# Optimization experiments

Measured on AMD Instinct MI355X. Metric: run time of the kernel, lower is better.

The kernel has to match this reference:

```python
import jax, jax.numpy as jnp
import numpy as np

DIM = 256
H = 56
W = 56
WS = 7          # window_size
SHIFT = 3       # shift_size = WS // 2
NH = 8          # num_heads
HID = 4 * DIM   # mlp hidden
EPS = 1e-5
N = WS * WS     # tokens per window


def _rel_coords_table():
    # SwinV2 continuous log-spaced relative coords, pretrained_window_size=0
    r = np.arange(-(WS - 1), WS, dtype=np.float32)
    t = np.stack(np.meshgrid(r, r, indexing='ij'), axis=-1)[None]  # (1, 2WS-1, 2WS-1, 2)
    t = t / (WS - 1) * 8.0
    t = np.sign(t) * np.log2(np.abs(t) + 1.0) / np.log2(8.0)
    return jnp.asarray(t, jnp.float32)


def _rel_pos_index():
    coords = np.stack(np.meshgrid(np.arange(WS), np.arange(WS), indexing='ij'))  # (2, WS, WS)
    cf = coords.reshape(2, -1)
    rel = (cf[:, :, None] - cf[:, None, :]).transpose(1, 2, 0).astype(np.int64)  # (N, N, 2)
    rel[..., 0] += WS - 1
    rel[..., 1] += WS - 1
    rel[..., 0] *= 2 * WS - 1
    return jnp.asarray(rel.sum(-1), jnp.int32)  # (N, N)


def _attn_mask():
    # shifted-window mask: -100 where tokens come from different image regions
    img = np.zeros((1, H, W, 1), np.float32)
    cnt = 0
    for hs in (slice(0, -WS), slice(-WS, -SHIFT), slice(-SHIFT, None)):
        for ws_ in (slice(0, -WS), slice(-WS, -SHIFT), slice(-SHIFT, None)):
            img[:, hs, ws_, :] = cnt
            cnt += 1
    mw = img.reshape(1, H // WS, WS, W // WS, WS, 1).transpose(0, 1, 3, 2, 4, 5).reshape(-1, N)
    m = mw[:, None, :] - mw[:, :, None]
    return jnp.asarray(np.where(m != 0, -100.0, 0.0).astype(np.float32))  # (nW, N, N)


def _win_partition(x):  # (B, H, W, C) -> (B*nW, N, C)
    B, _, _, C = x.shape
    x = x.reshape(B, H // WS, WS, W // WS, WS, C).transpose(0, 1, 3, 2, 4, 5)
    return x.reshape(-1, N, C)


def _win_reverse(w, B):  # (B*nW, N, C) -> (B, H, W, C)
    C = w.shape[-1]
    x = w.reshape(B, H // WS, W // WS, WS, WS, C).transpose(0, 1, 3, 2, 4, 5)
    return x.reshape(B, H, W, C)


def _ln(x, g, b):
    mu = jnp.mean(x, axis=-1, keepdims=True)
    var = jnp.mean(jnp.square(x - mu), axis=-1, keepdims=True)
    return (x - mu) * jax.lax.rsqrt(var + EPS) * g + b


def setup_inputs() -> dict:
    key = jax.random.key(0)
    ks = jax.random.split(key, 16)
    s = lambda fan: 1.0 / np.sqrt(fan)
    return {
        'x': jax.random.normal(ks[0], (16, H * W, DIM), jnp.float32),
        'norm1_w': jnp.ones((DIM,), jnp.float32),
        'norm1_b': jnp.zeros((DIM,), jnp.float32),
        'qkv_w': jax.random.normal(ks[1], (3 * DIM, DIM), jnp.float32) * s(DIM),
        'q_bias': jnp.zeros((DIM,), jnp.float32),
        'v_bias': jnp.zeros((DIM,), jnp.float32),
        'logit_scale': jnp.full((NH, 1, 1), np.log(10.0), jnp.float32),
        'cpb_w1': jax.random.normal(ks[2], (512, 2), jnp.float32) * s(2),
        'cpb_b1': jnp.zeros((512,), jnp.float32),
        'cpb_w2': jax.random.normal(ks[3], (NH, 512), jnp.float32) * s(512),
        'proj_w': jax.random.normal(ks[4], (DIM, DIM), jnp.float32) * s(DIM),
        'proj_b': jnp.zeros((DIM,), jnp.float32),
        'norm2_w': jnp.ones((DIM,), jnp.float32),
        'norm2_b': jnp.zeros((DIM,), jnp.float32),
        'fc1_w': jax.random.normal(ks[5], (HID, DIM), jnp.float32) * s(DIM),
        'fc1_b': jnp.zeros((HID,), jnp.float32),
        'fc2_w': jax.random.normal(ks[6], (DIM, HID), jnp.float32) * s(HID),
        'fc2_b': jnp.zeros((DIM,), jnp.float32),
    }


def reference(x, norm1_w, norm1_b, qkv_w, q_bias, v_bias, logit_scale,
              cpb_w1, cpb_b1, cpb_w2, proj_w, proj_b,
              norm2_w, norm2_b, fc1_w, fc1_b, fc2_w, fc2_b):
    B, L, C = x.shape
    hd = C // NH
    shortcut = x

    # cyclic shift + window partition
    xs = jnp.roll(x.reshape(B, H, W, C), (-SHIFT, -SHIFT), axis=(1, 2))
    xw = _win_partition(xs)  # (B*nW, N, C)

    # qkv with q/v bias, zero k bias (SwinV2)
    qkv_b = jnp.concatenate([q_bias, jnp.zeros_like(q_bias), v_bias])
    qkv = (xw @ qkv_w.T + qkv_b).reshape(-1, N, 3, NH, hd).transpose(2, 0, 3, 1, 4)
    q, k, v = qkv[0], qkv[1], qkv[2]  # (B*nW, NH, N, hd)

    # cosine attention with clamped learned logit scale
    qn = q / jnp.maximum(jnp.linalg.norm(q, axis=-1, keepdims=True), 1e-12)
    kn = k / jnp.maximum(jnp.linalg.norm(k, axis=-1, keepdims=True), 1e-12)
    scale = jnp.exp(jnp.minimum(logit_scale, jnp.log(jnp.asarray(100.0, x.dtype))))
    attn = jnp.einsum('whnd,whmd->whnm', qn, kn) * scale[None]

    # continuous relative position bias via cpb MLP
    t = _rel_coords_table()  # (1, 2WS-1, 2WS-1, 2)
    tbl = (jax.nn.relu(t @ cpb_w1.T + cpb_b1) @ cpb_w2.T).reshape(-1, NH)
    rpb = tbl[_rel_pos_index().reshape(-1)].reshape(N, N, NH).transpose(2, 0, 1)
    attn = attn + (16.0 * jax.nn.sigmoid(rpb))[None]

    # shifted-window mask
    mask = _attn_mask()  # (nW, N, N)
    nW = mask.shape[0]
    attn = attn.reshape(B, nW, NH, N, N) + mask[None, :, None]
    attn = jax.nn.softmax(attn, axis=-1).reshape(-1, NH, N, N)

    out = jnp.einsum('whnm,whmd->whnd', attn, v).transpose(0, 2, 1, 3).reshape(-1, N, C)
    out = out @ proj_w.T + proj_b

    # reverse windows + reverse shift (SwinV2 post-norm residual)
    xs = jnp.roll(_win_reverse(out, B), (SHIFT, SHIFT), axis=(1, 2)).reshape(B, L, C)
    x = shortcut + _ln(xs, norm1_w, norm1_b)

    # MLP with tanh-approx GELU (matches Triton kernel), post-norm residual
    hmid = jax.nn.gelu(x @ fc1_w.T + fc1_b, approximate=True)
    mlp = hmid @ fc2_w.T + fc2_b
    return x + _ln(mlp, norm2_w, norm2_b)
```

## Files before the change

### kernel.cpp

```cpp
#include <hip/hip_runtime.h>
#include <hip/hip_bf16.h>

typedef __attribute__((ext_vector_type(8))) short short8;
typedef __attribute__((ext_vector_type(4))) float f32x4;

union I4S8 { int4 i; short8 s; };

#if defined(__has_builtin)
#if __has_builtin(__builtin_amdgcn_global_load_lds)
#define HAVE_GLL 1
#endif
#endif

__device__ __forceinline__ unsigned short f2b(float f) {
  union { __hip_bfloat16 h; unsigned short u; } c;
  c.h = __float2bfloat16(f);
  return c.u;
}
__device__ __forceinline__ unsigned pk2(float a, float b) {
  union { __hip_bfloat162 h2; unsigned u; } c;
  c.h2 = __hip_bfloat162{__float2bfloat16(a), __float2bfloat16(b)};
  return c.u;
}
__device__ __forceinline__ float b2f(unsigned short h) {
  return __uint_as_float(((unsigned)h) << 16);
}
__device__ __forceinline__ float gelu_fast(float v) {
  float c2 = 1.5957691216057308f * (v + 0.044715f * v * v * v);
  return v / (1.0f + __expf(-c2));
}

__device__ __forceinline__ void stage8(const unsigned short* ga, unsigned short* lds_base,
                                       int lane) {
#ifdef HAVE_GLL
  __builtin_amdgcn_global_load_lds(
      (const __attribute__((address_space(1))) void*)ga,
      (__attribute__((address_space(3))) void*)lds_base, 16, 0, 0);
#else
  *(int4*)(lds_base + (lane >> 3) * 64 + (lane & 7) * 8) = *(const int4*)ga;
#endif
}

__global__ void k_misc(const float* __restrict__ logit_scale,
                       const float* __restrict__ w1, const float* __restrict__ b1,
                       const float* __restrict__ w2,
                       float* __restrict__ scales, float* __restrict__ tblg) {
  const int bb = blockIdx.x;
  const int t = threadIdx.x;
  if (bb == 169) {
    if (t < 8) scales[t] = expf(fminf(logit_scale[t], logf(100.0f)));
    return;
  }
  __shared__ float red[4][8];
  int a = bb / 13, b = bb % 13;
  float ra = (float)(a - 6) * (8.0f / 6.0f);
  float rb = (float)(b - 6) * (8.0f / 6.0f);
  float sa = (ra > 0.f) ? 1.f : ((ra < 0.f) ? -1.f : 0.f);
  float sb = (rb > 0.f) ? 1.f : ((rb < 0.f) ? -1.f : 0.f);
  float t0 = sa * log2f(fabsf(ra) + 1.0f) / 3.0f;
  float t1 = sb * log2f(fabsf(rb) + 1.0f) / 3.0f;
  float acc[8];
#pragma unroll
  for (int hh = 0; hh < 8; ++hh) acc[hh] = 0.f;
#pragma unroll
  for (int jj = 0; jj < 2; ++jj) {
    int j = t + jj * 256;
    float hv = fmaxf(w1[2 * j] * t0 + w1[2 * j + 1] * t1 + b1[j], 0.0f);
#pragma unroll
    for (int hh = 0; hh < 8; ++hh) acc[hh] += w2[hh * 512 + j] * hv;
  }
#pragma unroll
  for (int hh = 0; hh < 8; ++hh) {
    acc[hh] += __shfl_xor(acc[hh], 1);
    acc[hh] += __shfl_xor(acc[hh], 2);
    acc[hh] += __shfl_xor(acc[hh], 4);
    acc[hh] += __shfl_xor(acc[hh], 8);
    acc[hh] += __shfl_xor(acc[hh], 16);
    acc[hh] += __shfl_xor(acc[hh], 32);
  }
  if ((t & 63) == 0) {
#pragma unroll
    for (int hh = 0; hh < 8; ++hh) red[t >> 6][hh] = acc[hh];
  }
  __syncthreads();
  if (t < 8) tblg[bb * 8 + t] = red[0][t] + red[1][t] + red[2][t] + red[3][t];
}

__global__ void k_bias(const float* __restrict__ tblg, float* __restrict__ biasT) {
  int idx = blockIdx.x * 256 + threadIdx.x;
  int h = idx >> 12, rem = idx & 4095, k = rem >> 6, q = rem & 63;
  float v;
  if (k >= 49 || q >= 49) {
    v = -3.0e8f;
  } else {
    int e = (q / 7 - k / 7 + 6) * 13 + (q % 7 - k % 7 + 6);
    float r = tblg[e * 8 + h];
    v = 16.0f / (1.0f + expf(-r));
  }
  biasT[idx] = v;
}

__global__ void k_cvt(const float* __restrict__ qkv_w, const float* __restrict__ proj_w,
                      const float* __restrict__ fc1_w, const float* __restrict__ fc2_w,
                      unsigned short* __restrict__ wq, unsigned short* __restrict__ wp,
                      unsigned short* __restrict__ w1, unsigned short* __restrict__ w2) {
  int i = blockIdx.x * 256 + threadIdx.x;
  if (i < 196608) wq[i] = f2b(qkv_w[i]);
  else if (i < 262144) wp[i - 196608] = f2b(proj_w[i - 196608]);
  else if (i < 524288) w1[i - 262144] = f2b(fc1_w[i - 262144]);
  else w2[i - 524288] = f2b(fc2_w[i - 524288]);
}

__global__ void k_xprep(const float* __restrict__ x, unsigned short* __restrict__ xw) {
  int id = blockIdx.x * 256 + threadIdx.x;
  int row = id >> 5, c8 = (id & 31) << 3;
  int win = row / 49, r = row - win * 49;
  int b = win >> 6, wi = (win >> 3) & 7, wj = win & 7;
  int i = r / 7, j = r - i * 7;
  int ho = (wi * 7 + i + 3) % 56;
  int wo = (wj * 7 + j + 3) % 56;
  const float* src = x + (size_t)(b * 3136 + ho * 56 + wo) * 256 + c8;
  float4 f0 = *(const float4*)(src);
  float4 f1 = *(const float4*)(src + 4);
  int4 pk;
  pk.x = pk2(f0.x, f0.y);
  pk.y = pk2(f0.z, f0.w);
  pk.z = pk2(f1.x, f1.y);
  pk.w = pk2(f1.z, f1.w);
  *(int4*)(xw + (size_t)row * 256 + c8) = pk;
}

__global__ void k_xb(const float* __restrict__ x1, unsigned short* __restrict__ xb) {
  int id = blockIdx.x * 256 + threadIdx.x;
  size_t off = (size_t)id << 3;
  const float* src = x1 + off;
  float4 f0 = *(const float4*)(src);
  float4 f1 = *(const float4*)(src + 4);
  int4 pk;
  pk.x = pk2(f0.x, f0.y);
  pk.y = pk2(f0.z, f0.w);
  pk.z = pk2(f1.x, f1.y);
  pk.w = pk2(f1.z, f1.w);
  *(int4*)(xb + off) = pk;
}

__launch_bounds__(512)
__global__ void k_qkvg(const unsigned short* __restrict__ xw, const unsigned short* __restrict__ wq,
                       const float* __restrict__ q_bias, const float* __restrict__ v_bias,
                       const float* __restrict__ scales, unsigned short* __restrict__ qkv) {
  const int mb = blockIdx.x, nb = blockIdx.y;
  const int t = threadIdx.x, lane = t & 63, w = t >> 6;
  const int wm = w >> 2, wn = w & 3;
  const int l15 = lane & 15, g = lane >> 4, rj = g << 2;

  __shared__ __align__(16) unsigned short As[128 * 64];
  __shared__ __align__(16) unsigned short Bs[256 * 64];

  f32x4 acc[4][4];
#pragma unroll
  for (int mf = 0; mf < 4; ++mf)
#pragma unroll
    for (int nf = 0; nf < 4; ++nf) acc[mf][nf] = (f32x4){0.f, 0.f, 0.f, 0.f};

  const int rl = lane >> 3;
  const int ca = (lane & 7) ^ rl;

  for (int kb = 0; kb < 4; ++kb) {
    __syncthreads();
#pragma unroll
    for (int i = 0; i < 6; ++i) {
      int gidx = w * 6 + i;
      if (gidx < 16) {
        int r = gidx * 8 + rl;
        stage8(xw + (size_t)(mb * 128 + r) * 256 + kb * 64 + ca * 8, As + gidx * 8 * 64, lane);
      } else {
        int gb = gidx - 16;
        int r = gb * 8 + rl;
        stage8(wq + (size_t)(nb * 256 + r) * 256 + kb * 64 + ca * 8, Bs + gb * 8 * 64, lane);
      }
    }
    __syncthreads();
#pragma unroll
    for (int ks = 0; ks < 2; ++ks) {
      short8 a_[4], b_[4];
#pragma unroll
      for (int mf = 0; mf < 4; ++mf) {
        int R = wm * 64 + mf * 16 + l15;
        a_[mf] = *(const short8*)(As + R * 64 + (((ks * 4 + g) ^ (R & 7)) << 3));
      }
#pragma unroll
      for (int nf = 0; nf < 4; ++nf) {
        int R = wn * 64 + nf * 16 + l15;
        b_[nf] = *(const short8*)(Bs + R * 64 + (((ks * 4 + g) ^ (R & 7)) << 3));
      }
#pragma unroll
      for (int mf = 0; mf < 4; ++mf)
#pragma unroll
        for (int nf = 0; nf < 4; ++nf)
          acc[mf][nf] = __builtin_amdgcn_mfma_f32_16x16x32_bf16(a_[mf], b_[nf], acc[mf][nf], 0, 0, 0);
    }
  }

  const int which = nb;
  if (which != 1) {
    const float* bp = (which == 0) ? q_bias : v_bias;
#pragma unroll
    for (int nf = 0; nf < 4; ++nf) {
      float bias = bp[wn * 64 + nf * 16 + l15];
#pragma unroll
      for (int mf = 0; mf < 4; ++mf)
#pragma unroll
        for (int j = 0; j < 4; ++j) acc[mf][nf][j] += bias;
    }
  }
  if (which < 2) {
#pragma unroll
    for (int mf = 0; mf < 4; ++mf)
#pragma unroll
      for (int p = 0; p < 2; ++p)
#pragma unroll
        for (int j = 0; j < 4; ++j) {
          float ss = acc[mf][2*p][j] * acc[mf][2*p][j] + acc[mf][2*p+1][j] * acc[mf][2*p+1][j];
          ss += __shfl_xor(ss, 1); ss += __shfl_xor(ss, 2);
          ss += __shfl_xor(ss, 4); ss += __shfl_xor(ss, 8);
          float inv = 1.0f / fmaxf(sqrtf(ss), 1e-12f);
          if (which == 0) inv *= scales[wn * 2 + p];
          acc[mf][2*p][j] *= inv;
          acc[mf][2*p+1][j] *= inv;
        }
  }
#pragma unroll
  for (int mf = 0; mf < 4; ++mf)
#pragma unroll
    for (int j = 0; j < 4; ++j) {
      int row_g = mb * 128 + wm * 64 + mf * 16 + rj + j;
      int win = row_g / 49, r = row_g - win * 49;
      size_t base = (((size_t)win * 3 + which) * 8) * 1568;
#pragma unroll
      for (int nf = 0; nf < 4; ++nf) {
        int h = wn * 2 + (nf >> 1), d = (nf & 1) * 16 + l15;
        qkv[base + (size_t)h * 1568 + r * 32 + d] = f2b(acc[mf][nf][j]);
      }
    }
}

__launch_bounds__(256, 4)
__global__ void k_attn2(unsigned short* __restrict__ qkv, const float* __restrict__ biasT) {
  const int win = blockIdx.x;
  const int wi = (win >> 3) & 7, wj = win & 7;
  const int t = threadIdx.x, lane = t & 63, w = t >> 6;
  const int l15 = lane & 15, g = lane >> 4;
  const int kk8 = g << 3, rj = g << 2;

  __shared__ __align__(16) unsigned short VT8[8 * 32 * 72];

  const int vi = (wi == 7) ? 1 : 0, vj = (wj == 7) ? 1 : 0;

  for (int idx = t; idx < 392; idx += 256) {
    int h = idx / 49, r = idx % 49;
    const unsigned short* vp = qkv + ((((size_t)win * 3 + 2) * 8 + h) * 49 + r) * 32;
    unsigned short vv[32];
    *(int4*)(vv + 0)  = *(const int4*)(vp + 0);
    *(int4*)(vv + 8)  = *(const int4*)(vp + 8);
    *(int4*)(vv + 16) = *(const int4*)(vp + 16);
    *(int4*)(vv + 24) = *(const int4*)(vp + 24);
    unsigned short* dst = VT8 + h * 2304;
#pragma unroll
    for (int d = 0; d < 32; ++d) dst[d * 72 + r] = vv[d];
  }
  for (int idx = t; idx < 3840; idx += 256) {
    int h = idx / 480, rem = idx % 480, d = rem / 15, r = 49 + rem % 15;
    VT8[h * 2304 + d * 72 + r] = 0;
  }
  __syncthreads();

  const int sA = l15 + ((g & 1) << 5);
  const int sB = sA + 16;
  const bool hi = ((g >> 1) & 1) != 0;

  unsigned ob[2][8][2];
  for (int hh = 0; hh < 2; ++hh) {
    const int h = w + hh * 4;
    const float* bT = biasT + (size_t)h * 4096;
    f32x4 s[4][4];
#pragma unroll
    for (int mf = 0; mf < 4; ++mf)
#pragma unroll
      for (int nf = 0; nf < 4; ++nf)
#pragma unroll
        for (int j = 0; j < 4; ++j)
          s[mf][nf][j] = bT[(mf * 16 + rj + j) * 64 + nf * 16 + l15];
    if (vi | vj) {
      int rq[4];
#pragma unroll
      for (int nf = 0; nf < 4; ++nf) {
        int q = nf * 16 + l15, qi = q / 7, qj = q - qi * 7;
        int aq = vi ? (qi < 4 ? 1 : 2) : 0;
        int bq = vj ? (qj < 4 ? 1 : 2) : 0;
        rq[nf] = aq * 3 + bq;
      }
#pragma unroll
      for (int mf = 0; mf < 4; ++mf)
#pragma unroll
        for (int j = 0; j < 4; ++j) {
          int k = mf * 16 + rj + j, ki = k / 7, kj = k - ki * 7;
          int ak = vi ? (ki < 4 ? 1 : 2) : 0;
          int bk = vj ? (kj < 4 ? 1 : 2) : 0;
          int rk = ak * 3 + bk;
#pragma unroll
          for (int nf = 0; nf < 4; ++nf)
            if (rq[nf] != rk) s[mf][nf][j] -= 100.0f;
        }
    }
    const unsigned short* kp = qkv + (((size_t)win * 3 + 1) * 8 + h) * 1568;
    const unsigned short* qp = qkv + (((size_t)win * 3 + 0) * 8 + h) * 1568;
    short8 ka[4], qa[4];
#pragma unroll
    for (int f = 0; f < 4; ++f) {
      ka[f] = *(const short8*)(kp + (f * 16 + l15) * 32 + kk8);
      qa[f] = *(const short8*)(qp + (f * 16 + l15) * 32 + kk8);
    }
#pragma unroll
    for (int mf = 0; mf < 4; ++mf)
#pragma unroll
      for (int nf = 0; nf < 4; ++nf)
        s[mf][nf] = __builtin_amdgcn_mfma_f32_16x16x32_bf16(ka[mf], qa[nf], s[mf][nf], 0, 0, 0);

    unsigned D[4][4][2];
#pragma unroll
    for (int nf = 0; nf < 4; ++nf) {
      float m = -3.0e8f;
#pragma unroll
      for (int mf = 0; mf < 4; ++mf)
#pragma unroll
        for (int j = 0; j < 4; ++j) m = fmaxf(m, s[mf][nf][j]);
      m = fmaxf(m, __shfl_xor(m, 16));
      m = fmaxf(m, __shfl_xor(m, 32));
      float sum = 0.f;
#pragma unroll
      for (int mf = 0; mf < 4; ++mf)
#pragma unroll
        for (int j = 0; j < 4; ++j) {
          float e = __expf(s[mf][nf][j] - m);
          s[mf][nf][j] = e; sum += e;
        }
      sum += __shfl_xor(sum, 16);
      sum += __shfl_xor(sum, 32);
      float inv = 1.0f / sum;
#pragma unroll
      for (int mf = 0; mf < 4; ++mf) {
        D[mf][nf][0] = pk2(s[mf][nf][0] * inv, s[mf][nf][1] * inv);
        D[mf][nf][1] = pk2(s[mf][nf][2] * inv, s[mf][nf][3] * inv);
      }
    }

    f32x4 o[8];
#pragma unroll
    for (int i = 0; i < 8; ++i) o[i] = (f32x4){0.f, 0.f, 0.f, 0.f};
#pragma unroll
    for (int ks = 0; ks < 2; ++ks) {
      short8 vb[2];
#pragma unroll
      for (int dt = 0; dt < 2; ++dt)
        vb[dt] = *(const short8*)(VT8 + h * 2304 + (dt * 16 + l15) * 72 + ks * 32 + kk8);
#pragma unroll
      for (int qt = 0; qt < 4; ++qt) {
        int a0 = __shfl((int)D[2*ks+0][qt][0], sA), a1 = __shfl((int)D[2*ks+1][qt][0], sA);
        int b0 = __shfl((int)D[2*ks+0][qt][1], sA), b1 = __shfl((int)D[2*ks+1][qt][1], sA);
        int c0 = __shfl((int)D[2*ks+0][qt][0], sB), c1 = __shfl((int)D[2*ks+1][qt][0], sB);
        int e0 = __shfl((int)D[2*ks+0][qt][1], sB), e1 = __shfl((int)D[2*ks+1][qt][1], sB);
        I4S8 u;
        u.i.x = hi ? a1 : a0;
        u.i.y = hi ? b1 : b0;
        u.i.z = hi ? c1 : c0;
        u.i.w = hi ? e1 : e0;
#pragma unroll
        for (int dt = 0; dt < 2; ++dt)
          o[qt * 2 + dt] = __builtin_amdgcn_mfma_f32_16x16x32_bf16(u.s, vb[dt], o[qt * 2 + dt], 0, 0, 0);
      }
    }
#pragma unroll
    for (int f = 0; f < 8; ++f) {
      ob[hh][f][0] = pk2(o[f][0], o[f][1]);
      ob[hh][f][1] = pk2(o[f][2], o[f][3]);
    }
  }
  __syncthreads();

  unsigned short* Ow = qkv + (size_t)win * 37632;
#pragma unroll
  for (int hh = 0; hh < 2; ++hh) {
    int h = w + hh * 4;
#pragma unroll
    for (int qt = 0; qt < 4; ++qt)
#pragma unroll
      for (int j = 0; j < 4; ++j) {
        int q = qt * 16 + rj + j;
        if (q < 49) {
#pragma unroll
          for (int dt = 0; dt < 2; ++dt)
            Ow[q * 256 + h * 32 + dt * 16 + l15] =
                (unsigned short)(ob[hh][qt * 2 + dt][j >> 1] >> ((j & 1) * 16));
        }
      }
  }
}

__launch_bounds__(256)
__global__ void k_proj(const unsigned short* __restrict__ qkvO, const unsigned short* __restrict__ wp,
                       const float* __restrict__ proj_b, const float* __restrict__ n1w,
                       const float* __restrict__ n1b, const float* __restrict__ x,
                       float* __restrict__ x1) {
  const int mb = blockIdx.x;
  const int t = threadIdx.x, lane = t & 63, w = t >> 6;
  const int l15 = lane & 15, g = lane >> 4, rj = g << 2;

  __shared__ __align__(16) unsigned short As[64 * 64];
  __shared__ __align__(16) unsigned short Bs[256 * 64];

  f32x4 acc[16];
#pragma unroll
  for (int nf = 0; nf < 16; ++nf) acc[nf] = (f32x4){0.f, 0.f, 0.f, 0.f};

  const int rl = lane >> 3;
  const int ca = (lane & 7) ^ rl;

  for (int kb = 0; kb < 4; ++kb) {
    __syncthreads();
#pragma unroll
    for (int cc = 0; cc < 2; ++cc) {
      int rloc = w * 16 + cc * 8 + rl;
      int row_g = mb * 64 + rloc;
      int win = row_g / 49, r = row_g - win * 49;
      stage8(qkvO + (size_t)win * 37632 + r * 256 + kb * 64 + ca * 8,
             As + (w * 16 + cc * 8) * 64, lane);
    }
#pragma unroll
    for (int cc = 0; cc < 4; ++cc) {
      int rloc = w * 64 + cc * 8 + rl;
      stage8(wp + (size_t)rloc * 256 + kb * 64 + ca * 8, Bs + (w * 64 + cc * 8) * 64, lane);
      int rloc2 = rloc + 32;
      stage8(wp + (size_t)rloc2 * 256 + kb * 64 + ca * 8, Bs + (w * 64 + cc * 8 + 32) * 64, lane);
    }
    __syncthreads();
#pragma unroll
    for (int ks = 0; ks < 2; ++ks) {
      int R = w * 16 + l15;
      short8 a_ = *(const short8*)(As + R * 64 + (((ks * 4 + g) ^ (R & 7)) << 3));
      short8 b_[16];
#pragma unroll
      for (int nf = 0; nf < 16; ++nf) {
        int Rb = nf * 16 + l15;
        b_[nf] = *(const short8*)(Bs + Rb * 64 + (((ks * 4 + g) ^ (Rb & 7)) << 3));
      }
#pragma unroll
      for (int nf = 0; nf < 16; ++nf)
        acc[nf] = __builtin_amdgcn_mfma_f32_16x16x32_bf16(a_, b_[nf], acc[nf], 0, 0, 0);
    }
  }
#pragma unroll
  for (int nf = 0; nf < 16; ++nf) {
    float bias = proj_b[nf * 16 + l15];
#pragma unroll
    for (int j = 0; j < 4; ++j) acc[nf][j] += bias;
  }
#pragma unroll
  for (int j = 0; j < 4; ++j) {
    float s = 0.f, s2 = 0.f;
#pragma unroll
    for (int nf = 0; nf < 16; ++nf) {
      float v = acc[nf][j];
      s += v; s2 += v * v;
    }
    s += __shfl_xor(s, 1);  s += __shfl_xor(s, 2);  s += __shfl_xor(s, 4);  s += __shfl_xor(s, 8);
    s2 += __shfl_xor(s2, 1); s2 += __shfl_xor(s2, 2); s2 += __shfl_xor(s2, 4); s2 += __shfl_xor(s2, 8);
    float mu = s * (1.0f / 256.0f);
    float var = s2 * (1.0f / 256.0f) - mu * mu;
    float rs = rsqrtf(var + 1e-5f);
    int row_g = mb * 64 + w * 16 + rj + j;
    int win = row_g / 49, r = row_g - win * 49;
    int b = win >> 6, wi = (win >> 3) & 7, wj = win & 7;
    int i2 = r / 7, j2 = r - i2 * 7;
    int ho = (wi * 7 + i2 + 3) % 56, wo = (wj * 7 + j2 + 3) % 56;
    size_t base = (size_t)(b * 3136 + ho * 56 + wo) * 256;
#pragma unroll
    for (int nf = 0; nf < 16; ++nf) {
      int col = nf * 16 + l15;
      float xv = x[base + col];
      x1[base + col] = xv + (acc[nf][j] - mu) * rs * n1w[col] + n1b[col];
    }
  }
}

__launch_bounds__(256)
__global__ void k_fc1(const unsigned short* __restrict__ xb, const unsigned short* __restrict__ w1,
                      const float* __restrict__ b1, unsigned short* __restrict__ Hbuf, int r0) {
  const int mb = blockIdx.x, nb = blockIdx.y;
  const int t = threadIdx.x, lane = t & 63, w = t >> 6;
  const int wm = w >> 1, wn = w & 1;
  const int l15 = lane & 15, g = lane >> 4, rj = g << 2;

  __shared__ __align__(16) unsigned short As[128 * 64];
  __shared__ __align__(16) unsigned short Bs[128 * 64];

  f32x4 acc[4][4];
#pragma unroll
  for (int mf = 0; mf < 4; ++mf)
#pragma unroll
    for (int nf = 0; nf < 4; ++nf) acc[mf][nf] = (f32x4){0.f, 0.f, 0.f, 0.f};

  const int row_g0 = r0 + mb * 128;
  const int rl = lane >> 3;
  const int ca = (lane & 7) ^ rl;

  for (int kb = 0; kb < 4; ++kb) {
    __syncthreads();
#pragma unroll
    for (int cc = 0; cc < 4; ++cc) {
      int r = w * 32 + cc * 8 + rl;
      stage8(xb + (size_t)(row_g0 + r) * 256 + kb * 64 + ca * 8, As + (w * 32 + cc * 8) * 64, lane);
      stage8(w1 + (size_t)(nb * 128 + r) * 256 + kb * 64 + ca * 8, Bs + (w * 32 + cc * 8) * 64, lane);
    }
    __syncthreads();
#pragma unroll
    for (int ks = 0; ks < 2; ++ks) {
      short8 a_[4], b_[4];
#pragma unroll
      for (int mf = 0; mf < 4; ++mf) {
        int R = wm * 64 + mf * 16 + l15;
        a_[mf] = *(const short8*)(As + R * 64 + (((ks * 4 + g) ^ (R & 7)) << 3));
      }
#pragma unroll
      for (int nf = 0; nf < 4; ++nf) {
        int R = wn * 64 + nf * 16 + l15;
        b_[nf] = *(const short8*)(Bs + R * 64 + (((ks * 4 + g) ^ (R & 7)) << 3));
      }
#pragma unroll
      for (int mf = 0; mf < 4; ++mf)
#pragma unroll
        for (int nf = 0; nf < 4; ++nf)
          acc[mf][nf] = __builtin_amdgcn_mfma_f32_16x16x32_bf16(a_[mf], b_[nf], acc[mf][nf], 0, 0, 0);
    }
  }
#pragma unroll
  for (int mf = 0; mf < 4; ++mf)
#pragma unroll
    for (int nf = 0; nf < 4; ++nf) {
      int col = nb * 128 + wn * 64 + nf * 16 + l15;
      float bias = b1[col];
#pragma unroll
      for (int j = 0; j < 4; ++j) {
        int row = mb * 128 + wm * 64 + mf * 16 + rj + j;
        Hbuf[(size_t)row * 1024 + col] = f2b(gelu_fast(acc[mf][nf][j] + bias));
      }
    }
}

__launch_bounds__(512)
__global__ void k_fc2(const unsigned short* __restrict__ Hbuf, const unsigned short* __restrict__ w2,
                      const float* __restrict__ b2, const float* __restrict__ n2w,
                      const float* __restrict__ n2b, float* __restrict__ xio, int r0) {
  const int mb = blockIdx.x;
  const int t = threadIdx.x, lane = t & 63, w = t >> 6;
  const int l15 = lane & 15, g = lane >> 4, rj = g << 2;

  __shared__ __align__(16) unsigned short As[128 * 64];
  __shared__ __align__(16) unsigned short Bs[256 * 64];

  f32x4 acc[16];
#pragma unroll
  for (int nf = 0; nf < 16; ++nf) acc[nf] = (f32x4){0.f, 0.f, 0.f, 0.f};

  const int rl = lane >> 3;
  const int ca = (lane & 7) ^ rl;

  for (int kb = 0; kb < 16; ++kb) {
    __syncthreads();
#pragma unroll
    for (int cc = 0; cc < 2; ++cc) {
      int gidx = w * 2 + cc;
      int rloc = gidx * 8 + rl;
      stage8(Hbuf + (size_t)(mb * 128 + rloc) * 1024 + kb * 64 + ca * 8,
             As + gidx * 8 * 64, lane);
    }
#pragma unroll
    for (int cc = 0; cc < 4; ++cc) {
      int gidx = w * 4 + cc;
      int rloc = gidx * 8 + rl;
      stage8(w2 + (size_t)rloc * 1024 + kb * 64 + ca * 8, Bs + gidx * 8 * 64, lane);
    }
    __syncthreads();
#pragma unroll
    for (int ks = 0; ks < 2; ++ks) {
      int R = w * 16 + l15;
      short8 a_ = *(const short8*)(As + R * 64 + (((ks * 4 + g) ^ (R & 7)) << 3));
      short8 b_[16];
#pragma unroll
      for (int nf = 0; nf < 16; ++nf) {
        int Rb = nf * 16 + l15;
        b_[nf] = *(const short8*)(Bs + Rb * 64 + (((ks * 4 + g) ^ (Rb & 7)) << 3));
      }
#pragma unroll
      for (int nf = 0; nf < 16; ++nf)
        acc[nf] = __builtin_amdgcn_mfma_f32_16x16x32_bf16(a_, b_[nf], acc[nf], 0, 0, 0);
    }
  }
#pragma unroll
  for (int nf = 0; nf < 16; ++nf) {
    float bias = b2[nf * 16 + l15];
#pragma unroll
    for (int j = 0; j < 4; ++j) acc[nf][j] += bias;
  }
#pragma unroll
  for (int j = 0; j < 4; ++j) {
    float s = 0.f, s2 = 0.f;
#pragma unroll
    for (int nf = 0; nf < 16; ++nf) {
      float v = acc[nf][j];
      s += v; s2 += v * v;
    }
    s += __shfl_xor(s, 1);  s += __shfl_xor(s, 2);  s += __shfl_xor(s, 4);  s += __shfl_xor(s, 8);
    s2 += __shfl_xor(s2, 1); s2 += __shfl_xor(s2, 2); s2 += __shfl_xor(s2, 4); s2 += __shfl_xor(s2, 8);
    float mu = s * (1.0f / 256.0f);
    float var = s2 * (1.0f / 256.0f) - mu * mu;
    float rs = rsqrtf(var + 1e-5f);
    size_t base = (size_t)(r0 + mb * 128 + w * 16 + rj + j) * 256;
#pragma unroll
    for (int nf = 0; nf < 16; ++nf) {
      int col = nf * 16 + l15;
      float xv = xio[base + col];
      xio[base + col] = xv + (acc[nf][j] - mu) * rs * n2w[col] + n2b[col];
    }
  }
}

extern "C" void kernel_launch(void* const* d_in, const int* in_sizes, int n_in,
                              void* d_out, int out_size, void* d_ws, size_t ws_size,
                              hipStream_t stream) {
  const float* x           = (const float*)d_in[0];
  const float* norm1_w     = (const float*)d_in[1];
  const float* norm1_b     = (const float*)d_in[2];
  const float* qkv_w       = (const float*)d_in[3];
  const float* q_bias      = (const float*)d_in[4];
  const float* v_bias      = (const float*)d_in[5];
  const float* logit_scale = (const float*)d_in[6];
  const float* cpb_w1      = (const float*)d_in[7];
  const float* cpb_b1      = (const float*)d_in[8];
  const float* cpb_w2      = (const float*)d_in[9];
  const float* proj_w      = (const float*)d_in[10];
  const float* proj_b      = (const float*)d_in[11];
  const float* norm2_w     = (const float*)d_in[12];
  const float* norm2_b     = (const float*)d_in[13];
  const float* fc1_w       = (const float*)d_in[14];
  const float* fc1_b       = (const float*)d_in[15];
  const float* fc2_w       = (const float*)d_in[16];
  const float* fc2_b       = (const float*)d_in[17];

  char* ws = (char*)d_ws;
  float*          scales  = (float*)(ws + 0);
  float*          tblg    = (float*)(ws + 64);
  unsigned short* wq      = (unsigned short*)(ws + 8192);
  float*          biasT   = (float*)(ws + 8192);
  unsigned short* wp      = (unsigned short*)(ws + 401408);
  unsigned short* w1b     = (unsigned short*)(ws + 532480);
  unsigned short* w2b     = (unsigned short*)(ws + 1056768);
  unsigned short* qkvbuf  = (unsigned short*)(ws + 1581056);
  unsigned short* xb      = (unsigned short*)(ws + 1581056);
  unsigned short* Hbuf    = (unsigned short*)(ws + 27271168);
  float*          x1      = (float*)d_out;
  unsigned short* xw      = (unsigned short*)d_out;

  k_misc<<<dim3(170), dim3(256), 0, stream>>>(logit_scale, cpb_w1, cpb_b1, cpb_w2, scales, tblg);
  k_cvt<<<dim3(3072), dim3(256), 0, stream>>>(qkv_w, proj_w, fc1_w, fc2_w, wq, wp, w1b, w2b);
  k_xprep<<<dim3(6272), dim3(256), 0, stream>>>(x, xw);
  k_qkvg<<<dim3(392, 3), dim3(512), 0, stream>>>(xw, wq, q_bias, v_bias, scales, qkvbuf);
  k_bias<<<dim3(128), dim3(256), 0, stream>>>(tblg, biasT);
  k_attn2<<<dim3(1024), dim3(256), 0, stream>>>(qkvbuf, biasT);
  k_proj<<<dim3(784), dim3(256), 0, stream>>>(qkvbuf, wp, proj_b, norm1_w, norm1_b, x, x1);
  k_xb<<<dim3(6272), dim3(256), 0, stream>>>(x1, xb);

  const size_t need_1pass = 27271168ull + 102760448ull;
  if (ws_size >= need_1pass) {
    k_fc1<<<dim3(392, 8), dim3(256), 0, stream>>>(xb, w1b, fc1_b, Hbuf, 0);
    k_fc2<<<dim3(392), dim3(512), 0, stream>>>(Hbuf, w2b, fc2_b, norm2_w, norm2_b, x1, 0);
  } else {
    k_fc1<<<dim3(196, 8), dim3(256), 0, stream>>>(xb, w1b, fc1_b, Hbuf, 0);
    k_fc2<<<dim3(196), dim3(512), 0, stream>>>(Hbuf, w2b, fc2_b, norm2_w, norm2_b, x1, 0);
    k_fc1<<<dim3(196, 8), dim3(256), 0, stream>>>(xb, w1b, fc1_b, Hbuf, 25088);
    k_fc2<<<dim3(196), dim3(512), 0, stream>>>(Hbuf, w2b, fc2_b, norm2_w, norm2_b, x1, 25088);
  }
}
```

Measured before the change: 329.2 us.

## Double-buffer fc2 LDS tiles and halve block rows to 64

The fc2 GEMM+LayerNorm kernel now uses 256-thread blocks covering 64 rows, with twice as many blocks. Its shared-memory A and B tiles are double-buffered so the next K-slice loads while MFMAs run on the current one, leaving one barrier per iteration instead of two. The aim is to hide global-load latency and raise the number of blocks. The cost is more LDS per block (about 72KB), which may limit occupancy, and each block re-reads the full 256-wide weight tile for only 64 rows, doubling weight traffic.

After: 327.9 us. About the same (-0.4%).

```diff
diff --git a/kernel.cpp b/kernel.cpp
--- a/kernel.cpp
+++ b/kernel.cpp
@@ -556,7 +556,7 @@
     }
 }
 
-__launch_bounds__(512)
+__launch_bounds__(256)
 __global__ void k_fc2(const unsigned short* __restrict__ Hbuf, const unsigned short* __restrict__ w2,
                       const float* __restrict__ b2, const float* __restrict__ n2w,
                       const float* __restrict__ n2b, float* __restrict__ xio, int r0) {
@@ -564,8 +564,8 @@
   const int t = threadIdx.x, lane = t & 63, w = t >> 6;
   const int l15 = lane & 15, g = lane >> 4, rj = g << 2;
 
-  __shared__ __align__(16) unsigned short As[128 * 64];
-  __shared__ __align__(16) unsigned short Bs[256 * 64];
+  __shared__ __align__(16) unsigned short As[2][64 * 64];
+  __shared__ __align__(16) unsigned short Bs[2][256 * 64];
 
   f32x4 acc[16];
 #pragma unroll
@@ -574,37 +574,57 @@
   const int rl = lane >> 3;
   const int ca = (lane & 7) ^ rl;
 
+  {
+#pragma unroll
+    for (int cc = 0; cc < 2; ++cc) {
+      int rloc = w * 16 + cc * 8 + rl;
+      stage8(Hbuf + (size_t)(mb * 64 + rloc) * 1024 + ca * 8, As[0] + (w * 16 + cc * 8) * 64, lane);
+    }
+#pragma unroll
+    for (int cc = 0; cc < 4; ++cc) {
+      int rloc = w * 64 + cc * 8 + rl;
+      stage8(w2 + (size_t)rloc * 1024 + ca * 8, Bs[0] + (w * 64 + cc * 8) * 64, lane);
+      stage8(w2 + (size_t)(rloc + 32) * 1024 + ca * 8, Bs[0] + (w * 64 + cc * 8 + 32) * 64, lane);
+    }
+  }
+  __syncthreads();
+
+  int cur = 0;
   for (int kb = 0; kb < 16; ++kb) {
-    __syncthreads();
-#pragma unroll
-    for (int cc = 0; cc < 2; ++cc) {
-      int gidx = w * 2 + cc;
-      int rloc = gidx * 8 + rl;
-      stage8(Hbuf + (size_t)(mb * 128 + rloc) * 1024 + kb * 64 + ca * 8,
-             As + gidx * 8 * 64, lane);
-    }
-#pragma unroll
-    for (int cc = 0; cc < 4; ++cc) {
-      int gidx = w * 4 + cc;
-      int rloc = gidx * 8 + rl;
-      stage8(w2 + (size_t)rloc * 1024 + kb * 64 + ca * 8, Bs + gidx * 8 * 64, lane);
-    }
-    __syncthreads();
+    if (kb < 15) {
+      int kn = (kb + 1) * 64;
+#pragma unroll
+      for (int cc = 0; cc < 2; ++cc) {
+        int rloc = w * 16 + cc * 8 + rl;
+        stage8(Hbuf + (size_t)(mb * 64 + rloc) * 1024 + kn + ca * 8,
+               As[cur ^ 1] + (w * 16 + cc * 8) * 64, lane);
+      }
+#pragma unroll
+      for (int cc = 0; cc < 4; ++cc) {
+        int rloc = w * 64 + cc * 8 + rl;
+        stage8(w2 + (size_t)rloc * 1024 + kn + ca * 8, Bs[cur ^ 1] + (w * 64 + cc * 8) * 64, lane);
+        stage8(w2 + (size_t)(rloc + 32) * 1024 + kn + ca * 8,
+               Bs[cur ^ 1] + (w * 64 + cc * 8 + 32) * 64, lane);
+      }
+    }
 #pragma unroll
     for (int ks = 0; ks < 2; ++ks) {
       int R = w * 16 + l15;
-      short8 a_ = *(const short8*)(As + R * 64 + (((ks * 4 + g) ^ (R & 7)) << 3));
+      short8 a_ = *(const short8*)(As[cur] + R * 64 + (((ks * 4 + g) ^ (R & 7)) << 3));
       short8 b_[16];
 #pragma unroll
       for (int nf = 0; nf < 16; ++nf) {
         int Rb = nf * 16 + l15;
-        b_[nf] = *(const short8*)(Bs + Rb * 64 + (((ks * 4 + g) ^ (Rb & 7)) << 3));
+        b_[nf] = *(const short8*)(Bs[cur] + Rb * 64 + (((ks * 4 + g) ^ (Rb & 7)) << 3));
       }
 #pragma unroll
       for (int nf = 0; nf < 16; ++nf)
         acc[nf] = __builtin_amdgcn_mfma_f32_16x16x32_bf16(a_, b_[nf], acc[nf], 0, 0, 0);
     }
-  }
+    __syncthreads();
+    cur ^= 1;
+  }
+
 #pragma unroll
   for (int nf = 0; nf < 16; ++nf) {
     float bias = b2[nf * 16 + l15];
@@ -624,7 +644,7 @@
     float mu = s * (1.0f / 256.0f);
     float var = s2 * (1.0f / 256.0f) - mu * mu;
     float rs = rsqrtf(var + 1e-5f);
-    size_t base = (size_t)(r0 + mb * 128 + w * 16 + rj + j) * 256;
+    size_t base = (size_t)(r0 + mb * 64 + w * 16 + rj + j) * 256;
 #pragma unroll
     for (int nf = 0; nf < 16; ++nf) {
       int col = nf * 16 + l15;
@@ -682,11 +702,11 @@
   const size_t need_1pass = 27271168ull + 102760448ull;
   if (ws_size >= need_1pass) {
     k_fc1<<<dim3(392, 8), dim3(256), 0, stream>>>(xb, w1b, fc1_b, Hbuf, 0);
-    k_fc2<<<dim3(392), dim3(512), 0, stream>>>(Hbuf, w2b, fc2_b, norm2_w, norm2_b, x1, 0);
+    k_fc2<<<dim3(784), dim3(256), 0, stream>>>(Hbuf, w2b, fc2_b, norm2_w, norm2_b, x1, 0);
   } else {
     k_fc1<<<dim3(196, 8), dim3(256), 0, stream>>>(xb, w1b, fc1_b, Hbuf, 0);
-    k_fc2<<<dim3(196), dim3(512), 0, stream>>>(Hbuf, w2b, fc2_b, norm2_w, norm2_b, x1, 0);
+    k_fc2<<<dim3(392), dim3(256), 0, stream>>>(Hbuf, w2b, fc2_b, norm2_w, norm2_b, x1, 0);
     k_fc1<<<dim3(196, 8), dim3(256), 0, stream>>>(xb, w1b, fc1_b, Hbuf, 25088);
-    k_fc2<<<dim3(196), dim3(512), 0, stream>>>(Hbuf, w2b, fc2_b, norm2_w, norm2_b, x1, 25088);
-  }
-}
+    k_fc2<<<dim3(392), dim3(256), 0, stream>>>(Hbuf, w2b, fc2_b, norm2_w, norm2_b, x1, 25088);
+  }
+}
```
